# Kernel optimization log

Measured on AMD Instinct MI355X. Metric: run time of the kernel, lower is better.

## Reference

```python
import jax, jax.numpy as jnp
import numpy as np

SIGMA_INIT = 1000.0


def setup_inputs() -> dict:
    key = jax.random.key(0)
    k1, k2, k3 = jax.random.split(key, 3)
    B, M, D, S = 1024, 209, 12288, 2
    input_data = jax.random.normal(k1, (B, D), dtype=jnp.float32)
    center = jax.random.normal(k2, (M, D), dtype=jnp.float32)
    sigma = SIGMA_INIT * jnp.ones((M,), dtype=jnp.float32)
    W = 50.0 * jax.random.normal(k3, (S, M), dtype=jnp.float32)
    b = jnp.zeros((S,), dtype=jnp.float32)
    return {"input_data": input_data, "center": center, "sigma": sigma, "W": W, "b": b}


def reference(input_data, center, sigma, W, b):
    # Euclidean distance ||x_i - c_j|| via GEMM expansion (avoids [B,M,D] diff tensor)
    x2 = jnp.sum(input_data * input_data, axis=1, keepdims=True)        # [B,1]
    c2 = jnp.sum(center * center, axis=1)[None, :]                      # [1,M]
    d2 = x2 + c2 - 2.0 * (input_data @ center.T)                        # [B,M]
    dist = jnp.sqrt(jnp.maximum(d2, 0.0))
    # Note: original divides the (non-squared) norm by sigma^2, then exp(-.)
    radial = jnp.exp(-dist / (sigma * sigma)[None, :])                  # [B,M]
    return radial @ W.T + b                                             # [B,S]
```

## Files before the change

kernel.cpp:

```cpp
#include <hip/hip_runtime.h>
#include <hip/hip_bf16.h>
#include <stdint.h>

#define B_SZ 1024
#define M_SZ 209
#define MPAD 256
#define D_SZ 12288
#define KC   48
#define KCH  (D_SZ / KC)
#define BK   64
#define NIT  (KCH / BK)
#define NB   16
#define BT   64
#define SROW 224
#define SLROW (KC * SROW)

#define CBF_OFF  0u
#define XXP_OFF  (MPAD * D_SZ * 2)
#define CCP_OFF  (XXP_OFF + B_SZ * KC * 4)
#define SLAB_OFF (CCP_OFF + MPAD * 2 * 4)

typedef __attribute__((ext_vector_type(8)))  short short8;
typedef __attribute__((ext_vector_type(16))) float floatx16;

__device__ __forceinline__ uint32_t pk2(float lo, float hi) {
    union { __hip_bfloat162 h; uint32_t u; } cv;
    cv.h = __float22bfloat162_rn(float2{lo, hi});
    return cv.u;
}

__device__ __forceinline__ float bfbits2f(unsigned short u) {
    union { uint32_t u; float f; } cv;
    cv.u = ((uint32_t)u) << 16;
    return cv.f;
}

__device__ __forceinline__ void gload_lds16(const void* g, void* l) {
    __builtin_amdgcn_global_load_lds(
        (const __attribute__((address_space(1))) void*)g,
        (__attribute__((address_space(3))) void*)l, 16, 0, 0);
}

__global__ __launch_bounds__(256) void rbf_prep(
    const float* __restrict__ c, unsigned short* __restrict__ cbf,
    float* __restrict__ ccp)
{
    __shared__ float red[4];
    const int j = blockIdx.x >> 1, h = blockIdx.x & 1;
    const int t = threadIdx.x;
    const int base = h * (D_SZ / 2);
    unsigned short* dst = cbf + (size_t)j * D_SZ + base;
    float s = 0.f;
    if (j < M_SZ) {
        const float* src = c + (size_t)j * D_SZ + base;
        for (int i = t * 8; i < D_SZ / 2; i += 2048) {
            float4 v0 = *(const float4*)(src + i);
            float4 v1 = *(const float4*)(src + i + 4);
            s += v0.x*v0.x + v0.y*v0.y + v0.z*v0.z + v0.w*v0.w
               + v1.x*v1.x + v1.y*v1.y + v1.z*v1.z + v1.w*v1.w;
            uint4 w = { pk2(v0.x,v0.y), pk2(v0.z,v0.w), pk2(v1.x,v1.y), pk2(v1.z,v1.w) };
            *(uint4*)(dst + i) = w;
        }
    } else {
        uint4 zz = {0u, 0u, 0u, 0u};
        for (int i = t * 8; i < D_SZ / 2; i += 2048) *(uint4*)(dst + i) = zz;
    }
#pragma unroll
    for (int off = 32; off > 0; off >>= 1) s += __shfl_down(s, off);
    if ((t & 63) == 0) red[t >> 6] = s;
    __syncthreads();
    if (t == 0) ccp[j * 2 + h] = red[0] + red[1] + red[2] + red[3];
}

__global__ __launch_bounds__(256, 3) void rbf_main(
    const float* __restrict__ x, const unsigned short* __restrict__ cbf,
    __hip_bfloat16* __restrict__ slab, float* __restrict__ xxp)
{
    __shared__ unsigned short sx[BT * BK];
    __shared__ unsigned short sc[MPAD * BK];

    const int t    = threadIdx.x;
    const int k    = blockIdx.x;
    const int b    = blockIdx.y;
    const int wave = t >> 6, lane = t & 63;
    const int n = lane & 31, h = lane >> 5, e = lane & 7;
    const int rowtile = wave & 1;
    const int ctbase  = (wave >> 1) * 4;

    floatx16 acc[4];
#pragma unroll
    for (int i = 0; i < 4; ++i)
#pragma unroll
        for (int r2 = 0; r2 < 16; ++r2) acc[i][r2] = 0.f;

    const int r  = t >> 2;
    const int c0 = (t & 3) * 2;
    const float* xp = x + (size_t)(b * BT + r) * D_SZ + (size_t)k * KCH + (t & 3) * 16;

    uint4 xw[NIT][2];
    float sxx = 0.f;
#pragma unroll
    for (int it = 0; it < NIT; ++it) {
        float4 v0 = *(const float4*)(xp + it * BK + 0);
        float4 v1 = *(const float4*)(xp + it * BK + 4);
        float4 v2 = *(const float4*)(xp + it * BK + 8);
        float4 v3 = *(const float4*)(xp + it * BK + 12);
        sxx += v0.x*v0.x + v0.y*v0.y + v0.z*v0.z + v0.w*v0.w
             + v1.x*v1.x + v1.y*v1.y + v1.z*v1.z + v1.w*v1.w
             + v2.x*v2.x + v2.y*v2.y + v2.z*v2.z + v2.w*v2.w
             + v3.x*v3.x + v3.y*v3.y + v3.z*v3.z + v3.w*v3.w;
        xw[it][0] = make_uint4(pk2(v0.x,v0.y), pk2(v0.z,v0.w), pk2(v1.x,v1.y), pk2(v1.z,v1.w));
        xw[it][1] = make_uint4(pk2(v2.x,v2.y), pk2(v2.z,v2.w), pk2(v3.x,v3.y), pk2(v3.z,v3.w));
    }
    unsigned short* xw0 = &sx[r * BK + ((c0    ) ^ (r & 7)) * 8];
    unsigned short* xw1 = &sx[r * BK + ((c0 + 1) ^ (r & 7)) * 8];

    const int lr8 = lane >> 3, lc8 = lane & 7;
    const unsigned short* cpb = cbf + (size_t)lr8 * D_SZ + (size_t)k * KCH
                              + (size_t)((lc8 ^ lr8) * 8);

    const unsigned short* abase = &sx[(rowtile * 32 + n) * BK];
    const unsigned short* bbase = &sc[n * BK];

    for (int it = 0; it < NIT; ++it) {
#pragma unroll
        for (int jj = 0; jj < 8; ++jj) {
            const int cr = wave * 8 + jj;
            gload_lds16(cpb + (size_t)cr * 8 * D_SZ + it * BK, &sc[cr * 512]);
        }
        *(uint4*)xw0 = xw[it][0];
        *(uint4*)xw1 = xw[it][1];
        __syncthreads();

#pragma unroll
        for (int ks = 0; ks < 4; ++ks) {
            const int ch = (((2 * ks + h) ^ e)) * 8;
            short8 a = *(const short8*)(abase + ch);
#pragma unroll
            for (int cc2 = 0; cc2 < 4; ++cc2) {
                short8 bf = *(const short8*)(bbase + (ctbase + cc2) * 32 * BK + ch);
                acc[cc2] = __builtin_amdgcn_mfma_f32_32x32x16_bf16(a, bf, acc[cc2], 0, 0, 0);
            }
        }
        __syncthreads();
    }

    __hip_bfloat16* sd = slab + (size_t)k * SROW;
    const int gib = b * BT + rowtile * 32 + 4 * h;
#pragma unroll
    for (int cc2 = 0; cc2 < 4; ++cc2) {
        const int gj = (ctbase + cc2) * 32 + n;
        if (gj < SROW) {
#pragma unroll
            for (int reg = 0; reg < 16; ++reg) {
                const int gi = gib + (reg & 3) + 8 * (reg >> 2);
                sd[(size_t)gi * SLROW + gj] = __float2bfloat16(acc[cc2][reg]);
            }
        }
    }

    sxx += __shfl_down(sxx, 2);
    sxx += __shfl_down(sxx, 1);
    if ((t & 3) == 0) xxp[(size_t)(b * BT + r) * KC + k] = sxx;
}

__global__ __launch_bounds__(256) void rbf_fin(
    const __hip_bfloat16* __restrict__ slab, const float* __restrict__ xxp,
    const float* __restrict__ ccp, const float* __restrict__ sigma,
    const float* __restrict__ W, const float* __restrict__ bias,
    float* __restrict__ out)
{
    __shared__ float xsh;
    __shared__ float red[8];

    const int t = threadIdx.x;
    const int i = blockIdx.x;
    const int wave = t >> 6, lane = t & 63;

    float s = 0.f;
    if (t < SROW) {
        const unsigned short* sp = (const unsigned short*)slab + (size_t)i * SLROW + t;
#pragma unroll 8
        for (int kk = 0; kk < KC; ++kk) s += bfbits2f(sp[kk * SROW]);
    }

    if (t < 64) {
        float xv = (t < KC) ? xxp[(size_t)i * KC + t] : 0.f;
#pragma unroll
        for (int off = 32; off > 0; off >>= 1) xv += __shfl_down(xv, off);
        if (t == 0) xsh = xv;
    }
    __syncthreads();

    float a0 = 0.f, a1 = 0.f;
    if (t < M_SZ) {
        const float ccj = ccp[t * 2] + ccp[t * 2 + 1];
        float d2 = fmaxf(xsh + ccj - 2.f * s, 0.f);
        float sg = sigma[t];
        float rad = __expf(-sqrtf(d2) / (sg * sg));
        a0 = rad * W[t];
        a1 = rad * W[M_SZ + t];
    }
#pragma unroll
    for (int off = 32; off > 0; off >>= 1) {
        a0 += __shfl_down(a0, off);
        a1 += __shfl_down(a1, off);
    }
    if (lane == 0) { red[wave * 2] = a0; red[wave * 2 + 1] = a1; }
    __syncthreads();
    if (t == 0) out[i * 2 + 0] = red[0] + red[2] + red[4] + red[6] + bias[0];
    if (t == 1) out[i * 2 + 1] = red[1] + red[3] + red[5] + red[7] + bias[1];
}

extern "C" void kernel_launch(void* const* d_in, const int* in_sizes, int n_in,
                              void* d_out, int out_size, void* d_ws, size_t ws_size,
                              hipStream_t stream)
{
    const float* x     = (const float*)d_in[0];
    const float* c     = (const float*)d_in[1];
    const float* sigma = (const float*)d_in[2];
    const float* W     = (const float*)d_in[3];
    const float* bias  = (const float*)d_in[4];
    float* out = (float*)d_out;

    char* ws = (char*)d_ws;
    unsigned short*  cbf  = (unsigned short*)(ws + CBF_OFF);
    float*           xxp  = (float*)(ws + XXP_OFF);
    float*           ccp  = (float*)(ws + CCP_OFF);
    __hip_bfloat16*  slab = (__hip_bfloat16*)(ws + SLAB_OFF);

    rbf_prep<<<MPAD * 2, 256, 0, stream>>>(c, cbf, ccp);
    rbf_main<<<dim3(KC, NB), 256, 0, stream>>>(x, cbf, slab, xxp);
    rbf_fin<<<B_SZ, 256, 0, stream>>>(slab, xxp, ccp, sigma, W, bias, out);
}
```

Baseline: 116.1 us.

## Switch to 16x16 MFMA tiles, prefetch centers, store partial sums as fp8

The main kernel now uses 16x16x32 bf16 MFMA with each wave owning 16 rows across 14 column tiles. The padded center count drops from 256 to 224 so tiles past the live columns are skipped. The split-K count goes from 48 to 64, and the next center tile is prefetched into LDS right after the compute barrier. Partial dot products are written to the slab as fp8 instead of bf16, halving the traffic to and from the finishing kernel. The fp8 rounding of partial sums can produce large errors in d2 = x2 + c2 - 2xc, since that difference is cancellation-heavy, and the higher occupancy bound may cause register pressure.

Measured after the change: 123.7 us. 1.07x slower.

```diff
diff --git a/kernel.cpp b/kernel.cpp
--- a/kernel.cpp
+++ b/kernel.cpp
@@ -4,14 +4,15 @@
 
 #define B_SZ 1024
 #define M_SZ 209
-#define MPAD 256
+#define MPAD 224
 #define D_SZ 12288
-#define KC   48
+#define KC   64
 #define KCH  (D_SZ / KC)
 #define BK   64
 #define NIT  (KCH / BK)
 #define NB   16
 #define BT   64
+#define NCT  14
 #define SROW 224
 #define SLROW (KC * SROW)
 
@@ -20,8 +21,8 @@
 #define CCP_OFF  (XXP_OFF + B_SZ * KC * 4)
 #define SLAB_OFF (CCP_OFF + MPAD * 2 * 4)
 
-typedef __attribute__((ext_vector_type(8)))  short short8;
-typedef __attribute__((ext_vector_type(16))) float floatx16;
+typedef __attribute__((ext_vector_type(8))) short short8;
+typedef __attribute__((ext_vector_type(4))) float floatx4;
 
 __device__ __forceinline__ uint32_t pk2(float lo, float hi) {
     union { __hip_bfloat162 h; uint32_t u; } cv;
@@ -29,10 +30,9 @@
     return cv.u;
 }
 
-__device__ __forceinline__ float bfbits2f(unsigned short u) {
-    union { uint32_t u; float f; } cv;
-    cv.u = ((uint32_t)u) << 16;
-    return cv.f;
+__device__ __forceinline__ uint8_t f2fp8(float v) {
+    int p = __builtin_amdgcn_cvt_pk_fp8_f32(v, v, 0, false);
+    return (uint8_t)(p & 0xff);
 }
 
 __device__ __forceinline__ void gload_lds16(const void* g, void* l) {
@@ -72,9 +72,9 @@
     if (t == 0) ccp[j * 2 + h] = red[0] + red[1] + red[2] + red[3];
 }
 
-__global__ __launch_bounds__(256, 3) void rbf_main(
+__global__ __launch_bounds__(256, 4) void rbf_main(
     const float* __restrict__ x, const unsigned short* __restrict__ cbf,
-    __hip_bfloat16* __restrict__ slab, float* __restrict__ xxp)
+    uint8_t* __restrict__ slab, float* __restrict__ xxp)
 {
     __shared__ unsigned short sx[BT * BK];
     __shared__ unsigned short sc[MPAD * BK];
@@ -83,15 +83,23 @@
     const int k    = blockIdx.x;
     const int b    = blockIdx.y;
     const int wave = t >> 6, lane = t & 63;
-    const int n = lane & 31, h = lane >> 5, e = lane & 7;
-    const int rowtile = wave & 1;
-    const int ctbase  = (wave >> 1) * 4;
-
-    floatx16 acc[4];
-#pragma unroll
-    for (int i = 0; i < 4; ++i)
-#pragma unroll
-        for (int r2 = 0; r2 < 16; ++r2) acc[i][r2] = 0.f;
+    const int quad = lane >> 4, mrow = lane & 15;
+    const int m3   = mrow & 7;
+
+    floatx4 acc[NCT];
+    const floatx4 z4 = {0.f, 0.f, 0.f, 0.f};
+#pragma unroll
+    for (int i = 0; i < NCT; ++i) acc[i] = z4;
+
+    const int lr8 = lane >> 3, lc8 = lane & 7;
+    const unsigned short* cpb = cbf + (size_t)lr8 * D_SZ + (size_t)k * KCH
+                              + (size_t)((lc8 ^ lr8) * 8);
+
+#pragma unroll
+    for (int jj = 0; jj < 7; ++jj) {
+        const int cr = wave * 7 + jj;
+        gload_lds16(cpb + (size_t)cr * 8 * D_SZ, &sc[cr * 512]);
+    }
 
     const int r  = t >> 2;
     const int c0 = (t & 3) * 2;
@@ -115,48 +123,46 @@
     unsigned short* xw0 = &sx[r * BK + ((c0    ) ^ (r & 7)) * 8];
     unsigned short* xw1 = &sx[r * BK + ((c0 + 1) ^ (r & 7)) * 8];
 
-    const int lr8 = lane >> 3, lc8 = lane & 7;
-    const unsigned short* cpb = cbf + (size_t)lr8 * D_SZ + (size_t)k * KCH
-                              + (size_t)((lc8 ^ lr8) * 8);
-
-    const unsigned short* abase = &sx[(rowtile * 32 + n) * BK];
-    const unsigned short* bbase = &sc[n * BK];
-
+    const unsigned short* ax0 = &sx[(wave * 16 + mrow) * BK + ((quad    ) ^ m3) * 8];
+    const unsigned short* ax1 = &sx[(wave * 16 + mrow) * BK + ((quad + 4) ^ m3) * 8];
+    const unsigned short* bx0 = &sc[mrow * BK + ((quad    ) ^ m3) * 8];
+    const unsigned short* bx1 = &sc[mrow * BK + ((quad + 4) ^ m3) * 8];
+
+#pragma unroll
     for (int it = 0; it < NIT; ++it) {
-#pragma unroll
-        for (int jj = 0; jj < 8; ++jj) {
-            const int cr = wave * 8 + jj;
-            gload_lds16(cpb + (size_t)cr * 8 * D_SZ + it * BK, &sc[cr * 512]);
-        }
         *(uint4*)xw0 = xw[it][0];
         *(uint4*)xw1 = xw[it][1];
         __syncthreads();
 
 #pragma unroll
-        for (int ks = 0; ks < 4; ++ks) {
-            const int ch = (((2 * ks + h) ^ e)) * 8;
-            short8 a = *(const short8*)(abase + ch);
-#pragma unroll
-            for (int cc2 = 0; cc2 < 4; ++cc2) {
-                short8 bf = *(const short8*)(bbase + (ctbase + cc2) * 32 * BK + ch);
-                acc[cc2] = __builtin_amdgcn_mfma_f32_32x32x16_bf16(a, bf, acc[cc2], 0, 0, 0);
+        for (int ks = 0; ks < 2; ++ks) {
+            short8 a = *(const short8*)(ks ? ax1 : ax0);
+            const unsigned short* bb = ks ? bx1 : bx0;
+#pragma unroll
+            for (int ct = 0; ct < NCT; ++ct) {
+                short8 bf = *(const short8*)(bb + ct * 1024);
+                acc[ct] = __builtin_amdgcn_mfma_f32_16x16x32_bf16(a, bf, acc[ct], 0, 0, 0);
             }
         }
         __syncthreads();
-    }
-
-    __hip_bfloat16* sd = slab + (size_t)k * SROW;
-    const int gib = b * BT + rowtile * 32 + 4 * h;
-#pragma unroll
-    for (int cc2 = 0; cc2 < 4; ++cc2) {
-        const int gj = (ctbase + cc2) * 32 + n;
-        if (gj < SROW) {
-#pragma unroll
-            for (int reg = 0; reg < 16; ++reg) {
-                const int gi = gib + (reg & 3) + 8 * (reg >> 2);
-                sd[(size_t)gi * SLROW + gj] = __float2bfloat16(acc[cc2][reg]);
+
+        if (it + 1 < NIT) {
+#pragma unroll
+            for (int jj = 0; jj < 7; ++jj) {
+                const int cr = wave * 7 + jj;
+                gload_lds16(cpb + (size_t)cr * 8 * D_SZ + (it + 1) * BK, &sc[cr * 512]);
             }
         }
+    }
+
+    uint8_t* sd = slab + (size_t)k * SROW;
+    const int gi0 = b * BT + wave * 16 + quad * 4;
+#pragma unroll
+    for (int ct = 0; ct < NCT; ++ct) {
+        const int gj = ct * 16 + mrow;
+#pragma unroll
+        for (int rg = 0; rg < 4; ++rg)
+            sd[(size_t)(gi0 + rg) * SLROW + gj] = f2fp8(acc[ct][rg]);
     }
 
     sxx += __shfl_down(sxx, 2);
@@ -165,7 +171,7 @@
 }
 
 __global__ __launch_bounds__(256) void rbf_fin(
-    const __hip_bfloat16* __restrict__ slab, const float* __restrict__ xxp,
+    const uint8_t* __restrict__ slab, const float* __restrict__ xxp,
     const float* __restrict__ ccp, const float* __restrict__ sigma,
     const float* __restrict__ W, const float* __restrict__ bias,
     float* __restrict__ out)
@@ -179,13 +185,14 @@
 
     float s = 0.f;
     if (t < SROW) {
-        const unsigned short* sp = (const unsigned short*)slab + (size_t)i * SLROW + t;
+        const uint8_t* sp = slab + (size_t)i * SLROW + t;
 #pragma unroll 8
-        for (int kk = 0; kk < KC; ++kk) s += bfbits2f(sp[kk * SROW]);
+        for (int kk = 0; kk < KC; ++kk)
+            s += __builtin_amdgcn_cvt_f32_fp8((int)sp[kk * SROW], 0);
     }
 
     if (t < 64) {
-        float xv = (t < KC) ? xxp[(size_t)i * KC + t] : 0.f;
+        float xv = xxp[(size_t)i * KC + t];
 #pragma unroll
         for (int off = 32; off > 0; off >>= 1) xv += __shfl_down(xv, off);
         if (t == 0) xsh = xv;
@@ -224,10 +231,10 @@
     float* out = (float*)d_out;
 
     char* ws = (char*)d_ws;
-    unsigned short*  cbf  = (unsigned short*)(ws + CBF_OFF);
-    float*           xxp  = (float*)(ws + XXP_OFF);
-    float*           ccp  = (float*)(ws + CCP_OFF);
-    __hip_bfloat16*  slab = (__hip_bfloat16*)(ws + SLAB_OFF);
+    unsigned short* cbf  = (unsigned short*)(ws + CBF_OFF);
+    float*          xxp  = (float*)(ws + XXP_OFF);
+    float*          ccp  = (float*)(ws + CCP_OFF);
+    uint8_t*        slab = (uint8_t*)(ws + SLAB_OFF);
 
     rbf_prep<<<MPAD * 2, 256, 0, stream>>>(c, cbf, ccp);
     rbf_main<<<dim3(KC, NB), 256, 0, stream>>>(x, cbf, slab, xxp);
```
